# Performance work log

Hardware: AMD Instinct MI355X
Metric: run time of the kernel (lower is better)

## Reference

```python
import jax, jax.numpy as jnp
import numpy as np

B, N, DEG, D, C = 8, 50000, 16, 64, 128
E = N * DEG
NPER = N // B


def setup_inputs() -> dict:
    key = jax.random.key(0)
    ks = jax.random.split(key, 8)
    input_hidden = jax.random.normal(ks[0], (B, C), jnp.float32)
    F_n = jax.random.normal(ks[1], (N, D), jnp.float32)
    F_e = jax.random.normal(ks[2], (E, D), jnp.float32)
    # every node has in-degree DEG (matches DGL batched graph with all nodes receiving mail)
    dst = jnp.repeat(jnp.arange(N, dtype=jnp.int32), DEG)
    src = jax.random.randint(ks[3], (E,), 0, N, jnp.int32)
    node_graph = jnp.arange(N, dtype=jnp.int32) // NPER  # graph id per node
    edge_graph = node_graph[dst]                          # graph id per edge
    sc_in = 1.0 / np.sqrt(C)
    sc2d = 1.0 / np.sqrt(2 * D)
    W_in = jax.random.normal(ks[4], (D, C), jnp.float32) * sc_in      # input_proj
    W_obj = jax.random.normal(ks[5], (1, 2 * D), jnp.float32) * sc2d  # object_score
    W_rel = jax.random.normal(ks[6], (1, 2 * D), jnp.float32) * sc2d  # relation_score
    W_phi = jax.random.normal(ks[7], (D, 2 * D), jnp.float32) * sc2d  # linear_phi_node
    return dict(input_hidden=input_hidden, F_n=F_n, F_e=F_e, src=src, dst=dst,
                node_graph=node_graph, edge_graph=edge_graph,
                W_in=W_in, W_obj=W_obj, W_rel=W_rel, W_phi=W_phi)


def reference(input_hidden, F_n, F_e, src, dst, node_graph, edge_graph,
              W_in, W_obj, W_rel, W_phi):
    n = F_n.shape[0]
    b = input_hidden.shape[0]
    d = F_n.shape[-1]
    # h_t = input_proj(input_hidden), broadcast per graph to nodes/edges
    h = input_hidden @ W_in.T            # [B, D]
    h_n = h[node_graph]                  # [N, D]
    h_e = h[edge_graph]                  # [E, D]
    # per-node / per-edge attention logits (k_update_steps = 1)
    s_n = (jnp.concatenate([h_n, F_n], axis=-1) @ W_obj.T)[:, 0]  # [N]
    s_e = (jnp.concatenate([h_e, F_e], axis=-1) @ W_rel.T)[:, 0]  # [E]
    # mailbox: each edge delivers (F_n[src], s_n[src]) and (F_e, s_e) to dst
    scores = jnp.concatenate([s_n[src], s_e], axis=0)      # [2E]
    vals = jnp.concatenate([F_n[src], F_e], axis=0)        # [2E, D]
    seg = jnp.concatenate([dst, dst], axis=0)              # [2E]
    # ragged segment softmax over incoming messages per destination node
    m = jax.ops.segment_max(scores, seg, num_segments=n)
    ex = jnp.exp(scores - m[seg])
    denom = jax.ops.segment_sum(ex, seg, num_segments=n)   # [N]
    agg = jax.ops.segment_sum(vals * ex[:, None], seg, num_segments=n) / denom[:, None]
    # F_i_tplus1 = relu(linear_phi_node([applied_alpha, F_i]))
    F_new = jax.nn.relu(jnp.concatenate([agg, F_n], axis=-1) @ W_phi.T)  # [N, D]
    # equal-size graphs -> pad_sequence is a reshape
    io = F_new.reshape(b, n // b, d)
    io_mask = io.sum(axis=-1) != 0
    return io, io_mask
```

## Files before the change

### kernel.cpp

```cpp
#include <hip/hip_runtime.h>

#define BG   8
#define NN   50000
#define DEG  16
#define DD   64
#define CC   128


__global__ void k_setup(const float* __restrict__ IH, const float* __restrict__ W_in,
                        const float* __restrict__ W_obj, const float* __restrict__ W_rel,
                        float* __restrict__ ws) {
    int t = threadIdx.x;
    int g = t >> 6, d = t & 63;
    float acc = 0.f;
    #pragma unroll 8
    for (int c = 0; c < CC; ++c) acc += IH[g * CC + c] * W_in[d * CC + c];
    ws[t] = acc;
    __syncthreads();
    if (t < 16) {
        int gg = t & 7;
        const float* w = (t < 8) ? W_obj : W_rel;
        float s = 0.f;
        #pragma unroll 8
        for (int d2 = 0; d2 < DD; ++d2) s += ws[gg * DD + d2] * w[d2];
        ws[512 + t] = s;
    }
}

__global__ void k_sn(const float* __restrict__ F_n, const int* __restrict__ node_graph,
                     const float* __restrict__ W_obj, const float* __restrict__ ws,
                     float* __restrict__ s_n) {
    int i = blockIdx.x * blockDim.x + threadIdx.x;
    if (i >= NN) return;
    const float4* f4 = (const float4*)(F_n + (long)i * DD);
    const float4* w4 = (const float4*)(W_obj + DD);
    float acc = 0.f;
    #pragma unroll
    for (int k = 0; k < DD / 4; ++k) {
        float4 a = f4[k], b = w4[k];
        acc += a.x * b.x + a.y * b.y + a.z * b.z + a.w * b.w;
    }
    s_n[i] = acc + ws[512 + node_graph[i]];
}

__device__ __forceinline__ float wave_sum(float v) {
    #pragma unroll
    for (int off = 32; off; off >>= 1) v += __shfl_xor(v, off, 64);
    return v;
}

__global__ __launch_bounds__(256, 4) void k_main(
    const float* __restrict__ F_n, const float* __restrict__ F_e,
    const int* __restrict__ src, const int* __restrict__ node_graph,
    const float* __restrict__ W_rel, const float* __restrict__ W_phi,
    const float* __restrict__ ws, const float* __restrict__ s_n,
    float* __restrict__ out) {
    __shared__ float W2[DD][132];
    __shared__ float U[4][2 * DD];

    int tid = threadIdx.x;
    #pragma unroll
    for (int it = 0; it < 8; ++it) {
        int idx4 = (it * 256 + tid) * 4;
        float4 v = *(const float4*)(W_phi + idx4);
        int d = idx4 >> 7, c = idx4 & 127;
        *(float4*)&W2[d][c] = v;
    }

    int wave = tid >> 6, lane = tid & 63;
    int i = blockIdx.x * 4 + wave;
    const float wrel = W_rel[DD + lane];
    const long ibase = (long)i * DD;
    float fn_i = F_n[ibase + lane];
    const int eb = i * DEG;

    float fe[DEG];
    const float* fep = F_e + (long)eb * DD + lane;
    #pragma unroll
    for (int k = 0; k < DEG; ++k) fe[k] = fep[k * DD];

    float sn[DEG], fns[DEG];
    const int* sp = src + eb;
    #pragma unroll
    for (int k = 0; k < DEG; ++k) {
        int s = sp[k];
        sn[k] = s_n[s];
        fns[k] = F_n[(long)s * DD + lane];
    }

    float crel = ws[520 + node_graph[i]];
    float se[DEG];
    #pragma unroll
    for (int k = 0; k < DEG; ++k) {
        se[k] = wave_sum(fe[k] * wrel) + crel;
    }

    float m = -1e30f;
    #pragma unroll
    for (int k = 0; k < DEG; ++k) { m = fmaxf(m, se[k]); m = fmaxf(m, sn[k]); }
    float denom = 0.f, agg = 0.f;
    #pragma unroll
    for (int k = 0; k < DEG; ++k) {
        float en = __expf(sn[k] - m);
        denom += en;
        agg = fmaf(fns[k], en, agg);
        float ee = __expf(se[k] - m);
        denom += ee;
        agg = fmaf(fe[k], ee, agg);
    }
    agg /= denom;

    U[wave][lane] = agg;
    U[wave][DD + lane] = fn_i;
    __syncthreads();

    float acc = 0.f;
    #pragma unroll
    for (int c = 0; c < 2 * DD; c += 4) {
        float4 u4 = *(const float4*)&U[wave][c];
        float4 w4 = *(const float4*)&W2[lane][c];
        acc = fmaf(w4.x, u4.x, acc);
        acc = fmaf(w4.y, u4.y, acc);
        acc = fmaf(w4.z, u4.z, acc);
        acc = fmaf(w4.w, u4.w, acc);
    }
    acc = fmaxf(acc, 0.f);
    out[ibase + lane] = acc;

    float s = wave_sum(acc);
    if (lane == 0) out[(long)NN * DD + i] = (s != 0.f) ? 1.f : 0.f;
}

extern "C" void kernel_launch(void* const* d_in, const int* in_sizes, int n_in,
                              void* d_out, int out_size, void* d_ws, size_t ws_size,
                              hipStream_t stream) {
    const float* IH     = (const float*)d_in[0];
    const float* F_n    = (const float*)d_in[1];
    const float* F_e    = (const float*)d_in[2];
    const int*   src    = (const int*)d_in[3];
    const int*   ngr    = (const int*)d_in[5];
    const float* W_in   = (const float*)d_in[7];
    const float* W_obj  = (const float*)d_in[8];
    const float* W_rel  = (const float*)d_in[9];
    const float* W_phi  = (const float*)d_in[10];
    float* out = (float*)d_out;
    float* ws  = (float*)d_ws;
    float* s_n = ws + 528;

    k_setup<<<1, 512, 0, stream>>>(IH, W_in, W_obj, W_rel, ws);
    k_sn<<<(NN + 255) / 256, 256, 0, stream>>>(F_n, ngr, W_obj, ws, s_n);
    k_main<<<NN / 4, 256, 0, stream>>>(F_n, F_e, src, ngr, W_rel, W_phi, ws, s_n, out);
}
```

Before: 346.4 us.

## Process four nodes per wave to amortize W_phi LDS staging, swizzle LDS

Each wave now handles four destination nodes in a serial loop, so a block covers 16 nodes instead of 4. The 32KB W_phi staging into shared memory is therefore amortized over four times as many nodes, and the final matvec reuses each W row across four node vectors. W_phi is stored with an XOR swizzle instead of padding to avoid LDS bank conflicts. The gather loop uses '#pragma unroll 1', which reduces the loads in flight per wave and can hurt latency hiding in this memory-bound kernel. The grid also shrinks to 3125 blocks.

Result: slower. 888.5 us (+156.5%).

```diff
diff --git a/kernel.cpp b/kernel.cpp
--- a/kernel.cpp
+++ b/kernel.cpp
@@ -1,10 +1,11 @@
 #include <hip/hip_runtime.h>
 
-#define BG   8
 #define NN   50000
 #define DEG  16
 #define DD   64
 #define CC   128
+#define NPW  4
+#define NPB  16
 
 
 __global__ void k_setup(const float* __restrict__ IH, const float* __restrict__ W_in,
@@ -55,80 +56,89 @@
     const float* __restrict__ W_rel, const float* __restrict__ W_phi,
     const float* __restrict__ ws, const float* __restrict__ s_n,
     float* __restrict__ out) {
-    __shared__ float W2[DD][132];
-    __shared__ float U[4][2 * DD];
+    __shared__ float4 W2[DD * 32];
+    __shared__ float  U[4][NPW][2 * DD];
 
     int tid = threadIdx.x;
     #pragma unroll
     for (int it = 0; it < 8; ++it) {
-        int idx4 = (it * 256 + tid) * 4;
-        float4 v = *(const float4*)(W_phi + idx4);
-        int d = idx4 >> 7, c = idx4 & 127;
-        *(float4*)&W2[d][c] = v;
+        int s = it * 256 + tid;
+        int d = s >> 5, c4 = s & 31;
+        W2[d * 32 + (c4 ^ (d & 7))] = ((const float4*)W_phi)[s];
     }
 
     int wave = tid >> 6, lane = tid & 63;
-    int i = blockIdx.x * 4 + wave;
     const float wrel = W_rel[DD + lane];
-    const long ibase = (long)i * DD;
-    float fn_i = F_n[ibase + lane];
-    const int eb = i * DEG;
+    const int i0 = blockIdx.x * NPB + wave * NPW;
 
-    float fe[DEG];
-    const float* fep = F_e + (long)eb * DD + lane;
-    #pragma unroll
-    for (int k = 0; k < DEG; ++k) fe[k] = fep[k * DD];
+    #pragma unroll 1
+    for (int n = 0; n < NPW; ++n) {
+        const int i = i0 + n;
+        const long ibase = (long)i * DD;
+        const int eb = i * DEG;
 
-    float sn[DEG], fns[DEG];
-    const int* sp = src + eb;
-    #pragma unroll
-    for (int k = 0; k < DEG; ++k) {
-        int s = sp[k];
-        sn[k] = s_n[s];
-        fns[k] = F_n[(long)s * DD + lane];
+        float fe[DEG];
+        const float* fep = F_e + (long)eb * DD + lane;
+        #pragma unroll
+        for (int k = 0; k < DEG; ++k) fe[k] = fep[k * DD];
+
+        float sn[DEG], fns[DEG];
+        const int* sp = src + eb;
+        #pragma unroll
+        for (int k = 0; k < DEG; ++k) {
+            int sidx = sp[k];
+            sn[k] = s_n[sidx];
+            fns[k] = F_n[(long)sidx * DD + lane];
+        }
+
+        float crel = ws[520 + node_graph[i]];
+        float se[DEG];
+        #pragma unroll
+        for (int k = 0; k < DEG; ++k) se[k] = wave_sum(fe[k] * wrel) + crel;
+
+        float m = -1e30f;
+        #pragma unroll
+        for (int k = 0; k < DEG; ++k) { m = fmaxf(m, se[k]); m = fmaxf(m, sn[k]); }
+        float denom = 0.f, agg = 0.f;
+        #pragma unroll
+        for (int k = 0; k < DEG; ++k) {
+            float en = __expf(sn[k] - m);
+            denom += en;
+            agg = fmaf(fns[k], en, agg);
+            float ee = __expf(se[k] - m);
+            denom += ee;
+            agg = fmaf(fe[k], ee, agg);
+        }
+        agg /= denom;
+
+        U[wave][n][lane] = agg;
+        U[wave][n][DD + lane] = F_n[ibase + lane];
     }
 
-    float crel = ws[520 + node_graph[i]];
-    float se[DEG];
+    __syncthreads();
+
+    float acc[NPW] = {0.f, 0.f, 0.f, 0.f};
     #pragma unroll
-    for (int k = 0; k < DEG; ++k) {
-        se[k] = wave_sum(fe[k] * wrel) + crel;
+    for (int c4 = 0; c4 < 32; ++c4) {
+        float4 w4 = W2[lane * 32 + (c4 ^ (lane & 7))];
+        #pragma unroll
+        for (int n = 0; n < NPW; ++n) {
+            float4 u4 = *(const float4*)&U[wave][n][c4 * 4];
+            acc[n] = fmaf(w4.x, u4.x, acc[n]);
+            acc[n] = fmaf(w4.y, u4.y, acc[n]);
+            acc[n] = fmaf(w4.z, u4.z, acc[n]);
+            acc[n] = fmaf(w4.w, u4.w, acc[n]);
+        }
     }
 
-    float m = -1e30f;
     #pragma unroll
-    for (int k = 0; k < DEG; ++k) { m = fmaxf(m, se[k]); m = fmaxf(m, sn[k]); }
-    float denom = 0.f, agg = 0.f;
-    #pragma unroll
-    for (int k = 0; k < DEG; ++k) {
-        float en = __expf(sn[k] - m);
-        denom += en;
-        agg = fmaf(fns[k], en, agg);
-        float ee = __expf(se[k] - m);
-        denom += ee;
-        agg = fmaf(fe[k], ee, agg);
+    for (int n = 0; n < NPW; ++n) {
+        const int i = i0 + n;
+        float a = fmaxf(acc[n], 0.f);
+        out[(long)i * DD + lane] = a;
+        float ssum = wave_sum(a);
+        if (lane == 0) out[(long)NN * DD + i] = (ssum != 0.f) ? 1.f : 0.f;
     }
-    agg /= denom;
-
-    U[wave][lane] = agg;
-    U[wave][DD + lane] = fn_i;
-    __syncthreads();
-
-    float acc = 0.f;
-    #pragma unroll
-    for (int c = 0; c < 2 * DD; c += 4) {
-        float4 u4 = *(const float4*)&U[wave][c];
-        float4 w4 = *(const float4*)&W2[lane][c];
-        acc = fmaf(w4.x, u4.x, acc);
-        acc = fmaf(w4.y, u4.y, acc);
-        acc = fmaf(w4.z, u4.z, acc);
-        acc = fmaf(w4.w, u4.w, acc);
-    }
-    acc = fmaxf(acc, 0.f);
-    out[ibase + lane] = acc;
-
-    float s = wave_sum(acc);
-    if (lane == 0) out[(long)NN * DD + i] = (s != 0.f) ? 1.f : 0.f;
 }
 
 extern "C" void kernel_launch(void* const* d_in, const int* in_sizes, int n_in,
@@ -149,5 +159,5 @@
 
     k_setup<<<1, 512, 0, stream>>>(IH, W_in, W_obj, W_rel, ws);
     k_sn<<<(NN + 255) / 256, 256, 0, stream>>>(F_n, ngr, W_obj, ws, s_n);
-    k_main<<<NN / 4, 256, 0, stream>>>(F_n, F_e, src, ngr, W_rel, W_phi, ws, s_n, out);
+    k_main<<<NN / NPB, 256, 0, stream>>>(F_n, F_e, src, ngr, W_rel, W_phi, ws, s_n, out);
 }
```

## Compute edge scores with lane-parallel dot products and one-pass wave softmax

Applied to the files above, without the earlier changes.

Instead of 16 separate 64-lane butterfly reductions for the edge scores, each group of 4 lanes computes one edge's W_rel dot product from float4 loads, and a 2-step shuffle finishes it. The 32 message scores are then spread one per lane, so the max, exp and sum each take a single wave reduction, and the weights are broadcast by shuffle during aggregation. The W_phi shared-memory tile also drops its padding in favour of an XOR-swizzled float4 layout to avoid bank conflicts. This removes many shuffle and exp instructions, but F_e is now read twice (once strided, once as float4 for the scores) and the aggregation adds per-edge shuffles.

After: 364.3 us. 1.05x slower.

```diff
diff --git a/kernel.cpp b/kernel.cpp
--- a/kernel.cpp
+++ b/kernel.cpp
@@ -1,6 +1,5 @@
 #include <hip/hip_runtime.h>
 
-#define BG   8
 #define NN   50000
 #define DEG  16
 #define DD   64
@@ -43,82 +42,84 @@
     s_n[i] = acc + ws[512 + node_graph[i]];
 }
 
-__device__ __forceinline__ float wave_sum(float v) {
-    #pragma unroll
-    for (int off = 32; off; off >>= 1) v += __shfl_xor(v, off, 64);
-    return v;
-}
-
 __global__ __launch_bounds__(256, 4) void k_main(
     const float* __restrict__ F_n, const float* __restrict__ F_e,
     const int* __restrict__ src, const int* __restrict__ node_graph,
     const float* __restrict__ W_rel, const float* __restrict__ W_phi,
     const float* __restrict__ ws, const float* __restrict__ s_n,
     float* __restrict__ out) {
-    __shared__ float W2[DD][132];
-    __shared__ float U[4][2 * DD];
+    __shared__ float4 W2[DD * 32];
+    __shared__ float  U[4][2 * DD];
 
     int tid = threadIdx.x;
     #pragma unroll
     for (int it = 0; it < 8; ++it) {
-        int idx4 = (it * 256 + tid) * 4;
-        float4 v = *(const float4*)(W_phi + idx4);
-        int d = idx4 >> 7, c = idx4 & 127;
-        *(float4*)&W2[d][c] = v;
+        int s = it * 256 + tid;
+        int d = s >> 5, c4 = s & 31;
+        W2[d * 32 + (c4 ^ (d & 7))] = ((const float4*)W_phi)[s];
     }
 
-    int wave = tid >> 6, lane = tid & 63;
-    int i = blockIdx.x * 4 + wave;
-    const float wrel = W_rel[DD + lane];
+    const int wave = tid >> 6, lane = tid & 63;
+    const int i = blockIdx.x * 4 + wave;
     const long ibase = (long)i * DD;
-    float fn_i = F_n[ibase + lane];
     const int eb = i * DEG;
+    const int j = lane & 3, kq = lane >> 2;
+
+    float4 wr4[4];
+    #pragma unroll
+    for (int c = 0; c < 4; ++c) wr4[c] = ((const float4*)(W_rel + DD))[j * 4 + c];
 
     float fe[DEG];
     const float* fep = F_e + (long)eb * DD + lane;
     #pragma unroll
     for (int k = 0; k < DEG; ++k) fe[k] = fep[k * DD];
 
-    float sn[DEG], fns[DEG];
     const int* sp = src + eb;
+    float fns[DEG];
+    #pragma unroll
+    for (int k = 0; k < DEG; ++k) fns[k] = F_n[(long)sp[k] * DD + lane];
+
+    const float4* tp = (const float4*)(F_e + (long)eb * DD) + (kq * 16 + j * 4);
+    float p = 0.f;
+    #pragma unroll
+    for (int c = 0; c < 4; ++c) {
+        float4 a = tp[c], b = wr4[c];
+        p += a.x * b.x + a.y * b.y + a.z * b.z + a.w * b.w;
+    }
+    p += __shfl_xor(p, 1);
+    p += __shfl_xor(p, 2);
+
+    const float crel = ws[520 + node_graph[i]];
+    float se_b = __shfl(p, (lane & 15) * 4);
+    int   sidx_l = sp[lane & 15];
+    float sn_l = s_n[sidx_l];
+    float smsg = (lane < 16) ? (se_b + crel) : ((lane < 32) ? sn_l : -1e30f);
+
+    float M = smsg;
+    #pragma unroll
+    for (int off = 32; off; off >>= 1) M = fmaxf(M, __shfl_xor(M, off));
+    float em = (lane < 32) ? __expf(smsg - M) : 0.f;
+    float denom = em;
+    #pragma unroll
+    for (int off = 32; off; off >>= 1) denom += __shfl_xor(denom, off);
+
+    float agg = 0.f;
     #pragma unroll
     for (int k = 0; k < DEG; ++k) {
-        int s = sp[k];
-        sn[k] = s_n[s];
-        fns[k] = F_n[(long)s * DD + lane];
-    }
-
-    float crel = ws[520 + node_graph[i]];
-    float se[DEG];
-    #pragma unroll
-    for (int k = 0; k < DEG; ++k) {
-        se[k] = wave_sum(fe[k] * wrel) + crel;
-    }
-
-    float m = -1e30f;
-    #pragma unroll
-    for (int k = 0; k < DEG; ++k) { m = fmaxf(m, se[k]); m = fmaxf(m, sn[k]); }
-    float denom = 0.f, agg = 0.f;
-    #pragma unroll
-    for (int k = 0; k < DEG; ++k) {
-        float en = __expf(sn[k] - m);
-        denom += en;
-        agg = fmaf(fns[k], en, agg);
-        float ee = __expf(se[k] - m);
-        denom += ee;
-        agg = fmaf(fe[k], ee, agg);
+        agg = fmaf(fe[k],  __shfl(em, k), agg);
+        agg = fmaf(fns[k], __shfl(em, DEG + k), agg);
     }
     agg /= denom;
 
     U[wave][lane] = agg;
-    U[wave][DD + lane] = fn_i;
+    U[wave][DD + lane] = F_n[ibase + lane];
     __syncthreads();
 
     float acc = 0.f;
     #pragma unroll
-    for (int c = 0; c < 2 * DD; c += 4) {
-        float4 u4 = *(const float4*)&U[wave][c];
-        float4 w4 = *(const float4*)&W2[lane][c];
+    for (int c4 = 0; c4 < 32; ++c4) {
+        float4 w4 = W2[lane * 32 + (c4 ^ (lane & 7))];
+        float4 u4 = *(const float4*)&U[wave][c4 * 4];
         acc = fmaf(w4.x, u4.x, acc);
         acc = fmaf(w4.y, u4.y, acc);
         acc = fmaf(w4.z, u4.z, acc);
@@ -127,8 +128,10 @@
     acc = fmaxf(acc, 0.f);
     out[ibase + lane] = acc;
 
-    float s = wave_sum(acc);
-    if (lane == 0) out[(long)NN * DD + i] = (s != 0.f) ? 1.f : 0.f;
+    float ssum = acc;
+    #pragma unroll
+    for (int off = 32; off; off >>= 1) ssum += __shfl_xor(ssum, off);
+    if (lane == 0) out[(long)NN * DD + i] = (ssum != 0.f) ? 1.f : 0.f;
 }
 
 extern "C" void kernel_launch(void* const* d_in, const int* in_sizes, int n_in,
```
